# Performance work log

Hardware: AMD Instinct MI355X
Metric: run time of the kernel (lower is better)

The kernel has to match this reference:

```python
import jax, jax.numpy as jnp
import numpy as np

E, M, B, S = 1024, 256, 4, 2048
LN_EPS = 1e-5

def _l2norm(x):
    # F.normalize(p=2, dim=-1, eps=1e-12)
    n = jnp.linalg.norm(x, axis=-1, keepdims=True)
    return x / jnp.maximum(n, 1e-12)

def _layernorm(x, g, b):
    mu = jnp.mean(x, axis=-1, keepdims=True)
    var = jnp.var(x, axis=-1, keepdims=True)
    return (x - mu) * jax.lax.rsqrt(var + LN_EPS) * g + b

def setup_inputs() -> dict:
    key = jax.random.key(0)
    ks = jax.random.split(key, 16)
    s = 0.02
    inp = {
        'x': jax.random.normal(ks[0], (B, S, E), jnp.float32),
        'memory': jnp.zeros((B, M, M), jnp.float32),
        'w_k': jax.random.normal(ks[1], (M, E), jnp.float32) * s,
        'b_k': jnp.zeros((M,), jnp.float32),
        'w_q': jax.random.normal(ks[2], (M, E), jnp.float32) * s,
        'b_q': jnp.zeros((M,), jnp.float32),
        'w_v': jax.random.normal(ks[3], (M, E), jnp.float32) * s,
        'b_v': jnp.zeros((M,), jnp.float32),
        'w_out': jax.random.normal(ks[4], (E, M), jnp.float32) * s,
        'b_out': jnp.zeros((E,), jnp.float32),
        'w_gw': jax.random.normal(ks[5], (1, E), jnp.float32) * s,
        'b_gw': jnp.full((1,), -2.0, jnp.float32),
        'w_gf': jax.random.normal(ks[6], (1, E), jnp.float32) * s,
        'b_gf': jnp.full((1,), 2.0, jnp.float32),
        'ln1_g': jnp.ones((E,), jnp.float32),
        'ln1_b': jnp.zeros((E,), jnp.float32),
        'ln2_g': jnp.ones((E,), jnp.float32),
        'ln2_b': jnp.zeros((E,), jnp.float32),
        'w_f1': jax.random.normal(ks[7], (4 * E, E), jnp.float32) * s,
        'b_f1': jnp.zeros((4 * E,), jnp.float32),
        'w_f2': jax.random.normal(ks[8], (E, 4 * E), jnp.float32) * s,
        'b_f2': jnp.zeros((E,), jnp.float32),
    }
    return inp

def reference(x, memory, w_k, b_k, w_q, b_q, w_v, b_v, w_out, b_out,
              w_gw, b_gw, w_gf, b_gf, ln1_g, ln1_b, ln2_g, ln2_b,
              w_f1, b_f1, w_f2, b_f2):
    xn = _layernorm(x, ln1_g, ln1_b)                      # [B,S,E]
    k_all = _l2norm(xn @ w_k.T + b_k)                     # [B,S,M]
    q_all = _l2norm(xn @ w_q.T + b_q)                     # [B,S,M]
    v_all = jnp.tanh(xn @ w_v.T + b_v)                    # [B,S,M]
    beta_all = jax.nn.sigmoid(xn @ w_gw.T + b_gw)         # [B,S,1]
    decay_all = jax.nn.sigmoid(xn @ w_gf.T + b_gf)        # [B,S,1]

    def step(mem, inps):
        k, q, v, beta, decay = inps                       # k,q,v:[B,M]; beta,decay:[B,1]
        readout = jnp.einsum('bij,bj->bi', mem, q)        # read BEFORE update
        assoc = v[:, :, None] * k[:, None, :]             # [B,M,M] outer product
        mem = decay[:, :, None] * mem + beta[:, :, None] * assoc
        return mem, readout

    seq = (jnp.swapaxes(k_all, 0, 1), jnp.swapaxes(q_all, 0, 1),
           jnp.swapaxes(v_all, 0, 1), jnp.swapaxes(beta_all, 0, 1),
           jnp.swapaxes(decay_all, 0, 1))
    new_memory, readouts = jax.lax.scan(step, memory, seq)  # readouts: [S,B,M]
    stacked = jnp.swapaxes(readouts, 0, 1)                  # [B,S,M]
    mixer_out = stacked @ w_out.T + b_out                   # [B,S,E]

    x = x + mixer_out
    h = _layernorm(x, ln2_g, ln2_b)
    ffn = jax.nn.gelu(h @ w_f1.T + b_f1, approximate=False) @ w_f2.T + b_f2
    x = x + ffn
    return (x, new_memory)
```

## Files before the change

### kernel.cpp

```cpp
#include <hip/hip_runtime.h>
#include <stdint.h>

#define E_DIM 1024
#define M_DIM 256
#define B_DIM 4
#define S_DIM 2048
#define NTOK  8192
#define CHUNK 64
#define NCHUNK 32
#define NCB   128

typedef unsigned short u16;
typedef unsigned int   u32;
typedef __attribute__((ext_vector_type(8))) short short8;
typedef __attribute__((ext_vector_type(4))) float floatx4;

#define OFF_WKQV   ((size_t)0)
#define OFF_WOUT   ((size_t)1572864)
#define OFF_WF1    ((size_t)2097152)
#define OFF_WF2    ((size_t)10485760)
#define OFF_BKQV   ((size_t)18874368)
#define OFF_BETA   ((size_t)18877440)
#define OFF_DECAY  ((size_t)18910208)
#define OFF_P      ((size_t)18942976)
#define OFF_WW     ((size_t)18976256)
#define OFF_ABUF   ((size_t)19009024)
#define OFF_XN     ((size_t)21106176)
#define OFF_KQV    ((size_t)37883392)
#define OFF_T      ((size_t)63049216)
#define OFF_STATES ((size_t)96603648)
#define OFF_RO     ((size_t)130158080)
#define OFF_H      OFF_XN
#define OFF_Y1     OFF_T
#define OFF_G      OFF_STATES

__device__ __forceinline__ u16 f2bf(float f) {
    union { float f; u32 u; } a; a.f = f;
    u32 u = a.u;
    return (u16)((u + 0x7fffu + ((u >> 16) & 1u)) >> 16);
}
__device__ __forceinline__ u32 pack2bf(float a, float b) {
    return (u32)f2bf(a) | ((u32)f2bf(b) << 16);
}
__device__ __forceinline__ float sigmoidf_(float x) { return 1.0f / (1.0f + expf(-x)); }

__device__ __forceinline__ void gload_lds16(const u16* g, u16* l) {
    __builtin_amdgcn_global_load_lds((const __attribute__((address_space(1))) void*)g,
                                     (__attribute__((address_space(3))) void*)l, 16, 0, 0);
}

__device__ __forceinline__ int sw_slot(int idx) {
    return ((idx & 3) ^ ((idx >> 3) & 3)) * 8;
}
__device__ __forceinline__ int sw_read(int row, int kc) {
    return row * 32 + ((kc ^ ((row >> 1) & 3)) << 3);
}

__device__ __forceinline__ void block_reduce_2(float& a, float& b, float* red, int t) {
#pragma unroll
    for (int o = 32; o > 0; o >>= 1) { a += __shfl_xor(a, o); b += __shfl_xor(b, o); }
    if ((t & 63) == 0) { red[t >> 6] = a; red[4 + (t >> 6)] = b; }
    __syncthreads();
    a = red[0] + red[1] + red[2] + red[3];
    b = red[4] + red[5] + red[6] + red[7];
    __syncthreads();
}

__global__ void f2bf4_kernel(const float4* __restrict__ in, uint2* __restrict__ out, int n4) {
    int i = blockIdx.x * 256 + threadIdx.x;
    if (i < n4) {
        float4 v = in[i];
        uint2 o; o.x = pack2bf(v.x, v.y); o.y = pack2bf(v.z, v.w);
        out[i] = o;
    }
}
__global__ void pack_kqv_w(const float4* __restrict__ wk, const float4* __restrict__ wq,
                           const float4* __restrict__ wv, uint2* __restrict__ out) {
    int i = blockIdx.x * 256 + threadIdx.x;
    int sec = i >> 16;
    int off = i & 65535;
    const float4* src = (sec == 0) ? wk : ((sec == 1) ? wq : wv);
    float4 v = src[off];
    uint2 o; o.x = pack2bf(v.x, v.y); o.y = pack2bf(v.z, v.w);
    out[i] = o;
}
__global__ void pack_bias(const float* __restrict__ bk, const float* __restrict__ bq,
                          const float* __restrict__ bv, float* __restrict__ out) {
    int i = blockIdx.x * 256 + threadIdx.x;
    if (i < 256) out[i] = bk[i];
    else if (i < 512) out[i] = bq[i - 256];
    else out[i] = bv[i - 512];
}

__global__ __launch_bounds__(256) void ln1_gates(
    const float* __restrict__ x, const float* __restrict__ g, const float* __restrict__ b,
    const float* __restrict__ wgw, const float* __restrict__ bgw,
    const float* __restrict__ wgf, const float* __restrict__ bgf,
    u16* __restrict__ xn, float* __restrict__ beta, float* __restrict__ decay)
{
    __shared__ float red[8];
    const int row = blockIdx.x;
    const int t = threadIdx.x;
    const float4 v = ((const float4*)(x + (size_t)row * E_DIM))[t];
    float s  = v.x + v.y + v.z + v.w;
    float ss = v.x * v.x + v.y * v.y + v.z * v.z + v.w * v.w;
    block_reduce_2(s, ss, red, t);
    const float mean = s * (1.0f / E_DIM);
    const float var  = ss * (1.0f / E_DIM) - mean * mean;
    const float rstd = rsqrtf(var + 1e-5f);
    const float4 gg = ((const float4*)g)[t];
    const float4 bb = ((const float4*)b)[t];
    float4 xnv;
    xnv.x = (v.x - mean) * rstd * gg.x + bb.x;
    xnv.y = (v.y - mean) * rstd * gg.y + bb.y;
    xnv.z = (v.z - mean) * rstd * gg.z + bb.z;
    xnv.w = (v.w - mean) * rstd * gg.w + bb.w;
    uint2 o; o.x = pack2bf(xnv.x, xnv.y); o.y = pack2bf(xnv.z, xnv.w);
    ((uint2*)(xn + (size_t)row * E_DIM))[t] = o;
    const float4 w1 = ((const float4*)wgw)[t];
    const float4 w2 = ((const float4*)wgf)[t];
    float dg = xnv.x * w1.x + xnv.y * w1.y + xnv.z * w1.z + xnv.w * w1.w;
    float df = xnv.x * w2.x + xnv.y * w2.y + xnv.z * w2.z + xnv.w * w2.w;
    block_reduce_2(dg, df, red, t);
    if (t == 0) {
        beta[row]  = sigmoidf_(dg + bgw[0]);
        decay[row] = sigmoidf_(df + bgf[0]);
    }
}

__global__ __launch_bounds__(256) void ln2_kernel(
    const float* __restrict__ y1, const float* __restrict__ g, const float* __restrict__ b,
    u16* __restrict__ h)
{
    __shared__ float red[8];
    const int row = blockIdx.x;
    const int t = threadIdx.x;
    const float4 v = ((const float4*)(y1 + (size_t)row * E_DIM))[t];
    float s  = v.x + v.y + v.z + v.w;
    float ss = v.x * v.x + v.y * v.y + v.z * v.z + v.w * v.w;
    block_reduce_2(s, ss, red, t);
    const float mean = s * (1.0f / E_DIM);
    const float var  = ss * (1.0f / E_DIM) - mean * mean;
    const float rstd = rsqrtf(var + 1e-5f);
    const float4 gg = ((const float4*)g)[t];
    const float4 bb = ((const float4*)b)[t];
    float4 xnv;
    xnv.x = (v.x - mean) * rstd * gg.x + bb.x;
    xnv.y = (v.y - mean) * rstd * gg.y + bb.y;
    xnv.z = (v.z - mean) * rstd * gg.z + bb.z;
    xnv.w = (v.w - mean) * rstd * gg.w + bb.w;
    uint2 o; o.x = pack2bf(xnv.x, xnv.y); o.y = pack2bf(xnv.z, xnv.w);
    ((uint2*)(h + (size_t)row * E_DIM))[t] = o;
}

__global__ __launch_bounds__(256) void kqv_act(float* __restrict__ kqv) {
    __shared__ float red[8];
    const int row = blockIdx.x;
    const int t = threadIdx.x;
    float* p = kqv + (size_t)row * 768;
    float kv = p[t], qv = p[256 + t], vv = p[512 + t];
    float sk = kv * kv, sq = qv * qv;
    block_reduce_2(sk, sq, red, t);
    float nk = fmaxf(sqrtf(sk), 1e-12f);
    float nq = fmaxf(sqrtf(sq), 1e-12f);
    p[t]       = kv / nk;
    p[256 + t] = qv / nq;
    p[512 + t] = tanhf(vv);
}

__global__ void chunk_prep(const float* __restrict__ beta, const float* __restrict__ decay,
                           float* __restrict__ P, float* __restrict__ ww) {
    int cb = blockIdx.x;
    int b = cb >> 5, c = cb & 31;
    int tb = b * S_DIM + c * CHUNK;
    int j = threadIdx.x;
    __shared__ float d[64], bt[64], Ps[65];
    d[j]  = decay[tb + j];
    bt[j] = beta[tb + j];
    __syncthreads();
    if (j == 0) {
        float p = 1.0f; Ps[0] = 1.0f;
        for (int i = 0; i < 64; i++) { p *= d[i]; Ps[i + 1] = p; }
    }
    __syncthreads();
    P[cb * 65 + j] = Ps[j];
    if (j == 0) P[cb * 65 + 64] = Ps[64];
    ww[cb * 64 + j] = bt[j] / Ps[j + 1];
}

__global__ __launch_bounds__(256) void t_kernel(const float* __restrict__ kqv,
                                                const float* __restrict__ P,
                                                const float* __restrict__ ww,
                                                float* __restrict__ T) {
    int cb = blockIdx.y;
    int tile = blockIdx.x;
    int r0 = (tile >> 2) * 64, c0 = (tile & 3) * 64;
    int b = cb >> 5, c = cb & 31;
    int tb = b * S_DIM + c * CHUNK;
    float p64 = P[cb * 65 + 64];
    __shared__ float Vs[64][65], Ks[64][65];
    int t = threadIdx.x;
#pragma unroll
    for (int i = 0; i < 16; i++) {
        int idx = t + i * 256; int j = idx >> 6, col = idx & 63;
        float sc = ww[cb * 64 + j] * p64;
        Vs[j][col] = kqv[(size_t)(tb + j) * 768 + 512 + r0 + col] * sc;
        Ks[j][col] = kqv[(size_t)(tb + j) * 768 + 0   + c0 + col];
    }
    __syncthreads();
    int tr = t >> 4, tc = t & 15;
    float a[4][4] = {};
    for (int j = 0; j < 64; j++) {
        float vv[4], kk[4];
#pragma unroll
        for (int r = 0; r < 4; r++)  vv[r] = Vs[j][tr * 4 + r];
#pragma unroll
        for (int cc = 0; cc < 4; cc++) kk[cc] = Ks[j][tc * 4 + cc];
#pragma unroll
        for (int r = 0; r < 4; r++)
#pragma unroll
            for (int cc = 0; cc < 4; cc++) a[r][cc] += vv[r] * kk[cc];
    }
#pragma unroll
    for (int r = 0; r < 4; r++)
#pragma unroll
        for (int cc = 0; cc < 4; cc++)
            T[(size_t)cb * 65536 + (size_t)(r0 + tr * 4 + r) * 256 + (c0 + tc * 4 + cc)] = a[r][cc];
}

__global__ void mem_scan(const float* __restrict__ mem0, const float* __restrict__ T,
                         const float* __restrict__ P, float* __restrict__ states,
                         float* __restrict__ memOut) {
    int gid = blockIdx.x * 256 + threadIdx.x;
    int b = gid >> 16; int e = gid & 65535;
    float s = mem0[gid];
    for (int c = 0; c < NCHUNK; c++) {
        int cb = b * NCHUNK + c;
        states[(size_t)cb * 65536 + e] = s;
        s = P[cb * 65 + 64] * s + T[(size_t)cb * 65536 + e];
    }
    memOut[gid] = s;
}

__global__ __launch_bounds__(256) void qk_attn(const float* __restrict__ kqv,
                                               const float* __restrict__ P,
                                               const float* __restrict__ ww,
                                               float* __restrict__ Abuf) {
    int cb = blockIdx.x;
    int b = cb >> 5, c = cb & 31;
    int tb = b * S_DIM + c * CHUNK;
    __shared__ float Qs[64][65], Ks[64][65];
    int t = threadIdx.x;
    int tr = t >> 4, tc = t & 15;
    float acc[4][4] = {};
    for (int kt = 0; kt < 4; kt++) {
        __syncthreads();
#pragma unroll
        for (int i = 0; i < 16; i++) {
            int idx = t + i * 256; int rr = idx >> 6, cc2 = idx & 63;
            Qs[rr][cc2] = kqv[(size_t)(tb + rr) * 768 + 256 + kt * 64 + cc2];
            Ks[rr][cc2] = kqv[(size_t)(tb + rr) * 768 + 0   + kt * 64 + cc2];
        }
        __syncthreads();
        for (int kk = 0; kk < 64; kk++) {
            float qq[4], kx[4];
#pragma unroll
            for (int r = 0; r < 4; r++)  qq[r] = Qs[tr * 4 + r][kk];
#pragma unroll
            for (int cc = 0; cc < 4; cc++) kx[cc] = Ks[tc * 4 + cc][kk];
#pragma unroll
            for (int r = 0; r < 4; r++)
#pragma unroll
                for (int cc = 0; cc < 4; cc++) acc[r][cc] += qq[r] * kx[cc];
        }
    }
#pragma unroll
    for (int r = 0; r < 4; r++) {
#pragma unroll
        for (int cc = 0; cc < 4; cc++) {
            int i = tr * 4 + r, j = tc * 4 + cc;
            float v = (j < i) ? acc[r][cc] * (P[cb * 65 + i] * ww[cb * 64 + j]) : 0.0f;
            Abuf[(size_t)cb * 4096 + i * 64 + j] = v;
        }
    }
}

__global__ __launch_bounds__(256) void readout_k(const float* __restrict__ kqv,
                                                 const float* __restrict__ Abuf,
                                                 const float* __restrict__ states,
                                                 const float* __restrict__ P,
                                                 u16* __restrict__ ro) {
    int cb = blockIdx.y;
    int rt = blockIdx.x;
    int b = cb >> 5, c = cb & 31;
    int tb = b * S_DIM + c * CHUNK;
    int r0 = rt * 64;
    __shared__ float As[64][65], Vs[64][65], Qs[64][65], Ms[64][65];
    int t = threadIdx.x;
    int tr = t >> 4, tc = t & 15;
#pragma unroll
    for (int i = 0; i < 16; i++) {
        int idx = t + i * 256; int rr = idx >> 6, cc2 = idx & 63;
        As[rr][cc2] = Abuf[(size_t)cb * 4096 + rr * 64 + cc2];
        Vs[rr][cc2] = kqv[(size_t)(tb + rr) * 768 + 512 + r0 + cc2];
    }
    __syncthreads();
    float acc[4][4] = {};
    for (int j = 0; j < 64; j++) {
        float aa[4], vv[4];
#pragma unroll
        for (int r = 0; r < 4; r++)  aa[r] = As[tr * 4 + r][j];
#pragma unroll
        for (int cc = 0; cc < 4; cc++) vv[cc] = Vs[j][tc * 4 + cc];
#pragma unroll
        for (int r = 0; r < 4; r++)
#pragma unroll
            for (int cc = 0; cc < 4; cc++) acc[r][cc] += aa[r] * vv[cc];
    }
    float acc2[4][4] = {};
    for (int kt = 0; kt < 4; kt++) {
        __syncthreads();
#pragma unroll
        for (int i = 0; i < 16; i++) {
            int idx = t + i * 256; int rr = idx >> 6, cc2 = idx & 63;
            Qs[rr][cc2] = kqv[(size_t)(tb + rr) * 768 + 256 + kt * 64 + cc2];
            Ms[rr][cc2] = states[(size_t)cb * 65536 + (size_t)(r0 + rr) * 256 + kt * 64 + cc2];
        }
        __syncthreads();
        for (int kk = 0; kk < 64; kk++) {
            float qq[4], mm[4];
#pragma unroll
            for (int r = 0; r < 4; r++)  qq[r] = Qs[tr * 4 + r][kk];
#pragma unroll
            for (int cc = 0; cc < 4; cc++) mm[cc] = Ms[tc * 4 + cc][kk];
#pragma unroll
            for (int r = 0; r < 4; r++)
#pragma unroll
                for (int cc = 0; cc < 4; cc++) acc2[r][cc] += qq[r] * mm[cc];
        }
    }
#pragma unroll
    for (int r = 0; r < 4; r++) {
#pragma unroll
        for (int cc = 0; cc < 4; cc++) {
            int i = tr * 4 + r;
            float val = acc[r][cc] + P[cb * 65 + i] * acc2[r][cc];
            ro[(size_t)(tb + i) * 256 + r0 + tc * 4 + cc] = f2bf(val);
        }
    }
}

#define EPI_BIAS  0
#define EPI_RESID 1
#define EPI_GELU  2

template<int EPI, int BM>
__global__ __launch_bounds__(256) void gemm_bt(
    const u16* __restrict__ A, int lda,
    const u16* __restrict__ B, int ldb,
    const float* __restrict__ bias,
    const float* __restrict__ resid,
    float* __restrict__ outF, u16* __restrict__ outB,
    int ldc, int K)
{
    constexpr int MI = BM / 32;
    __shared__ u16 As[2][BM * 32];
    __shared__ u16 Bs[2][128 * 32];
    const int t = threadIdx.x;
    const int lane = t & 63;
    const int w = t >> 6;
    const int waveM = (w >> 1) * (BM / 2);
    const int waveN = (w & 1) * 64;
    const int m0 = blockIdx.y * BM;
    const int n0 = blockIdx.x * 128;

    const int sr = t >> 2, scw = sw_slot(t);
    const u16* Ag0 = A + (size_t)(m0 + sr) * lda + scw;
    const u16* Ag1 = A + (size_t)(m0 + 64 + sr) * lda + scw;
    const u16* Bg0 = B + (size_t)(n0 + sr) * ldb + scw;
    const u16* Bg1 = B + (size_t)(n0 + 64 + sr) * ldb + scw;

    floatx4 acc[MI][4] = {};

    const int kc = lane >> 4;
    const int rsel = lane & 15;
    const int NK = K >> 5;

    gload_lds16(Ag0, As[0] + t * 8);
    if (BM == 128) gload_lds16(Ag1, As[0] + (t + 256) * 8);
    gload_lds16(Bg0, Bs[0] + t * 8);
    gload_lds16(Bg1, Bs[0] + (t + 256) * 8);

    for (int kt = 0; kt < NK; kt++) {
        __syncthreads();
        const int cur = kt & 1;
        if (kt + 1 < NK) {
            const int kof = (kt + 1) * 32;
            gload_lds16(Ag0 + kof, As[cur ^ 1] + t * 8);
            if (BM == 128) gload_lds16(Ag1 + kof, As[cur ^ 1] + (t + 256) * 8);
            gload_lds16(Bg0 + kof, Bs[cur ^ 1] + t * 8);
            gload_lds16(Bg1 + kof, Bs[cur ^ 1] + (t + 256) * 8);
        }
        short8 af[MI], bfr[4];
#pragma unroll
        for (int i = 0; i < MI; i++)
            af[i] = *(const short8*)(As[cur] + sw_read(waveM + i * 16 + rsel, kc));
#pragma unroll
        for (int j = 0; j < 4; j++)
            bfr[j] = *(const short8*)(Bs[cur] + sw_read(waveN + j * 16 + rsel, kc));
#pragma unroll
        for (int i = 0; i < MI; i++)
#pragma unroll
            for (int j = 0; j < 4; j++)
                acc[i][j] = __builtin_amdgcn_mfma_f32_16x16x32_bf16(af[i], bfr[j], acc[i][j], 0, 0, 0);
    }

    const int rbase = (lane >> 4) * 4;
#pragma unroll
    for (int i = 0; i < MI; i++) {
#pragma unroll
        for (int j = 0; j < 4; j++) {
            const int col = n0 + waveN + j * 16 + rsel;
            const float bv = bias[col];
#pragma unroll
            for (int r = 0; r < 4; r++) {
                const int row = m0 + waveM + i * 16 + rbase + r;
                const size_t oidx = (size_t)row * ldc + col;
                float v = acc[i][j][r] + bv;
                if (EPI == EPI_BIAS) {
                    outF[oidx] = v;
                } else if (EPI == EPI_RESID) {
                    outF[oidx] = v + resid[oidx];
                } else {
                    float gl = 0.5f * v * (1.0f + erff(v * 0.70710678118654752f));
                    outB[oidx] = f2bf(gl);
                }
            }
        }
    }
}

extern "C" void kernel_launch(void* const* d_in, const int* in_sizes, int n_in,
                              void* d_out, int out_size, void* d_ws, size_t ws_size,
                              hipStream_t stream) {
    const float* x     = (const float*)d_in[0];
    const float* mem0  = (const float*)d_in[1];
    const float* w_k   = (const float*)d_in[2];
    const float* b_k   = (const float*)d_in[3];
    const float* w_q   = (const float*)d_in[4];
    const float* b_q   = (const float*)d_in[5];
    const float* w_v   = (const float*)d_in[6];
    const float* b_v   = (const float*)d_in[7];
    const float* w_out = (const float*)d_in[8];
    const float* b_out = (const float*)d_in[9];
    const float* w_gw  = (const float*)d_in[10];
    const float* b_gw  = (const float*)d_in[11];
    const float* w_gf  = (const float*)d_in[12];
    const float* b_gf  = (const float*)d_in[13];
    const float* ln1g  = (const float*)d_in[14];
    const float* ln1b  = (const float*)d_in[15];
    const float* ln2g  = (const float*)d_in[16];
    const float* ln2b  = (const float*)d_in[17];
    const float* w_f1  = (const float*)d_in[18];
    const float* b_f1  = (const float*)d_in[19];
    const float* w_f2  = (const float*)d_in[20];
    const float* b_f2  = (const float*)d_in[21];

    char* ws = (char*)d_ws;
    u16*   wkqv  = (u16*)(ws + OFF_WKQV);
    u16*   wout  = (u16*)(ws + OFF_WOUT);
    u16*   wf1   = (u16*)(ws + OFF_WF1);
    u16*   wf2   = (u16*)(ws + OFF_WF2);
    float* bkqv  = (float*)(ws + OFF_BKQV);
    float* beta  = (float*)(ws + OFF_BETA);
    float* decay = (float*)(ws + OFF_DECAY);
    float* P     = (float*)(ws + OFF_P);
    float* ww    = (float*)(ws + OFF_WW);
    float* Abuf  = (float*)(ws + OFF_ABUF);
    u16*   xn    = (u16*)(ws + OFF_XN);
    float* kqv   = (float*)(ws + OFF_KQV);
    float* T     = (float*)(ws + OFF_T);
    float* states= (float*)(ws + OFF_STATES);
    u16*   ro    = (u16*)(ws + OFF_RO);
    u16*   h     = (u16*)(ws + OFF_H);
    float* y1    = (float*)(ws + OFF_Y1);
    u16*   g     = (u16*)(ws + OFF_G);

    float* out_x   = (float*)d_out;
    float* out_mem = out_x + (size_t)NTOK * E_DIM;

    pack_kqv_w<<<768, 256, 0, stream>>>((const float4*)w_k, (const float4*)w_q,
                                        (const float4*)w_v, (uint2*)wkqv);
    f2bf4_kernel<<<256, 256, 0, stream>>>((const float4*)w_out, (uint2*)wout, 1024 * 256 / 4);
    f2bf4_kernel<<<4096, 256, 0, stream>>>((const float4*)w_f1, (uint2*)wf1, 4096 * 1024 / 4);
    f2bf4_kernel<<<4096, 256, 0, stream>>>((const float4*)w_f2, (uint2*)wf2, 1024 * 4096 / 4);
    pack_bias<<<3, 256, 0, stream>>>(b_k, b_q, b_v, bkqv);

    ln1_gates<<<NTOK, 256, 0, stream>>>(x, ln1g, ln1b, w_gw, b_gw, w_gf, b_gf, xn, beta, decay);

    gemm_bt<EPI_BIAS, 64><<<dim3(6, 128), 256, 0, stream>>>(xn, 1024, wkqv, 1024, bkqv, nullptr,
                                                            kqv, nullptr, 768, 1024);
    kqv_act<<<NTOK, 256, 0, stream>>>(kqv);

    chunk_prep<<<NCB, 64, 0, stream>>>(beta, decay, P, ww);
    t_kernel<<<dim3(16, NCB), 256, 0, stream>>>(kqv, P, ww, T);
    mem_scan<<<1024, 256, 0, stream>>>(mem0, T, P, states, out_mem);
    qk_attn<<<NCB, 256, 0, stream>>>(kqv, P, ww, Abuf);
    readout_k<<<dim3(4, NCB), 256, 0, stream>>>(kqv, Abuf, states, P, ro);

    gemm_bt<EPI_RESID, 64><<<dim3(8, 128), 256, 0, stream>>>(ro, 256, wout, 256, b_out, x,
                                                             y1, nullptr, 1024, 256);
    ln2_kernel<<<NTOK, 256, 0, stream>>>(y1, ln2g, ln2b, h);
    gemm_bt<EPI_GELU, 128><<<dim3(32, 64), 256, 0, stream>>>(h, 1024, wf1, 1024, b_f1, nullptr,
                                                             nullptr, g, 4096, 1024);
    gemm_bt<EPI_RESID, 64><<<dim3(8, 128), 256, 0, stream>>>(g, 4096, wf2, 4096, b_f2, y1,
                                                             out_x, nullptr, 1024, 4096);
}
```

Measured before the change: 531.4 us.

## Split-K the KQV and FFN2 GEMMs with larger tiles and merge weight conversions

Fuses the five weight/bias conversion launches into one kernel. The KQV projection and the second FFN GEMM now use 128-row tiles and a split-K of 2 across blockIdx.z. The second partial sum goes to scratch and is added back later: in kqv_act, which also applies the bias, or in a new combine kernel for the FFN output. This keeps enough blocks in flight with the larger tiles, at the cost of extra partial-sum traffic through global memory and one more launch.

```diff
diff --git a/kernel.cpp b/kernel.cpp
--- a/kernel.cpp
+++ b/kernel.cpp
@@ -33,6 +33,7 @@
 #define OFF_H      OFF_XN
 #define OFF_Y1     OFF_T
 #define OFF_G      OFF_STATES
+#define OFF_P2     OFF_XN
 
 __device__ __forceinline__ u16 f2bf(float f) {
     union { float f; u32 u; } a; a.f = f;
@@ -66,30 +67,35 @@
     __syncthreads();
 }
 
-__global__ void f2bf4_kernel(const float4* __restrict__ in, uint2* __restrict__ out, int n4) {
-    int i = blockIdx.x * 256 + threadIdx.x;
-    if (i < n4) {
-        float4 v = in[i];
-        uint2 o; o.x = pack2bf(v.x, v.y); o.y = pack2bf(v.z, v.w);
-        out[i] = o;
-    }
-}
-__global__ void pack_kqv_w(const float4* __restrict__ wk, const float4* __restrict__ wq,
-                           const float4* __restrict__ wv, uint2* __restrict__ out) {
-    int i = blockIdx.x * 256 + threadIdx.x;
-    int sec = i >> 16;
-    int off = i & 65535;
-    const float4* src = (sec == 0) ? wk : ((sec == 1) ? wq : wv);
-    float4 v = src[off];
-    uint2 o; o.x = pack2bf(v.x, v.y); o.y = pack2bf(v.z, v.w);
-    out[i] = o;
-}
-__global__ void pack_bias(const float* __restrict__ bk, const float* __restrict__ bq,
-                          const float* __restrict__ bv, float* __restrict__ out) {
-    int i = blockIdx.x * 256 + threadIdx.x;
-    if (i < 256) out[i] = bk[i];
-    else if (i < 512) out[i] = bq[i - 256];
-    else out[i] = bv[i - 512];
+__device__ __forceinline__ uint2 cvt4(float4 v) {
+    uint2 o; o.x = pack2bf(v.x, v.y); o.y = pack2bf(v.z, v.w); return o;
+}
+__global__ void convert_weights(const float4* __restrict__ wk, const float4* __restrict__ wq,
+                                const float4* __restrict__ wv, const float4* __restrict__ wo,
+                                const float4* __restrict__ wf1in, const float4* __restrict__ wf2in,
+                                const float* __restrict__ bk, const float* __restrict__ bq,
+                                const float* __restrict__ bv,
+                                uint2* __restrict__ wkqv, uint2* __restrict__ wout,
+                                uint2* __restrict__ wf1, uint2* __restrict__ wf2,
+                                float* __restrict__ bkqv) {
+    int b = blockIdx.x, t = threadIdx.x;
+    if (b < 768) {
+        int i = b * 256 + t;
+        int sec = i >> 16, off = i & 65535;
+        const float4* s = (sec == 0) ? wk : ((sec == 1) ? wq : wv);
+        wkqv[i] = cvt4(s[off]);
+    } else if (b < 1024) {
+        int i = (b - 768) * 256 + t;
+        wout[i] = cvt4(wo[i]);
+    } else if (b < 5120) {
+        int i = (b - 1024) * 256 + t;
+        wf1[i] = cvt4(wf1in[i]);
+    } else if (b < 9216) {
+        int i = (b - 5120) * 256 + t;
+        wf2[i] = cvt4(wf2in[i]);
+    } else {
+        bkqv[t] = bk[t]; bkqv[256 + t] = bq[t]; bkqv[512 + t] = bv[t];
+    }
 }
 
 __global__ __launch_bounds__(256) void ln1_gates(
@@ -153,12 +159,17 @@
     ((uint2*)(h + (size_t)row * E_DIM))[t] = o;
 }
 
-__global__ __launch_bounds__(256) void kqv_act(float* __restrict__ kqv) {
+__global__ __launch_bounds__(256) void kqv_act(float* __restrict__ pA,
+                                               const float* __restrict__ pB,
+                                               const float* __restrict__ bias) {
     __shared__ float red[8];
     const int row = blockIdx.x;
     const int t = threadIdx.x;
-    float* p = kqv + (size_t)row * 768;
-    float kv = p[t], qv = p[256 + t], vv = p[512 + t];
+    float* p = pA + (size_t)row * 768;
+    const float* q = pB + (size_t)row * 768;
+    float kv = p[t]       + q[t]       + bias[t];
+    float qv = p[256 + t] + q[256 + t] + bias[256 + t];
+    float vv = p[512 + t] + q[512 + t] + bias[512 + t];
     float sk = kv * kv, sq = qv * qv;
     block_reduce_2(sk, sq, red, t);
     float nk = fmaxf(sqrtf(sk), 1e-12f);
@@ -350,9 +361,19 @@
     }
 }
 
-#define EPI_BIAS  0
-#define EPI_RESID 1
-#define EPI_GELU  2
+__global__ __launch_bounds__(256) void combine_k(float4* __restrict__ out,
+                                                 const float4* __restrict__ part) {
+    int i = blockIdx.x * 256 + threadIdx.x;
+    float4 a = out[i], b = part[i];
+    a.x += b.x; a.y += b.y; a.z += b.z; a.w += b.w;
+    out[i] = a;
+}
+
+#define EPI_BIAS   0
+#define EPI_RESID  1
+#define EPI_GELU   2
+#define EPI_SPART  3
+#define EPI_SRESID 4
 
 template<int EPI, int BM>
 __global__ __launch_bounds__(256) void gemm_bt(
@@ -361,7 +382,7 @@
     const float* __restrict__ bias,
     const float* __restrict__ resid,
     float* __restrict__ outF, u16* __restrict__ outB,
-    int ldc, int K)
+    int ldc, int K, float* __restrict__ part)
 {
     constexpr int MI = BM / 32;
     __shared__ u16 As[2][BM * 32];
@@ -373,12 +394,13 @@
     const int waveN = (w & 1) * 64;
     const int m0 = blockIdx.y * BM;
     const int n0 = blockIdx.x * 128;
+    const size_t koff = (size_t)blockIdx.z * K;
 
     const int sr = t >> 2, scw = sw_slot(t);
-    const u16* Ag0 = A + (size_t)(m0 + sr) * lda + scw;
-    const u16* Ag1 = A + (size_t)(m0 + 64 + sr) * lda + scw;
-    const u16* Bg0 = B + (size_t)(n0 + sr) * ldb + scw;
-    const u16* Bg1 = B + (size_t)(n0 + 64 + sr) * ldb + scw;
+    const u16* Ag0 = A + (size_t)(m0 + sr) * lda + koff + scw;
+    const u16* Ag1 = A + (size_t)(m0 + 64 + sr) * lda + koff + scw;
+    const u16* Bg0 = B + (size_t)(n0 + sr) * ldb + koff + scw;
+    const u16* Bg1 = B + (size_t)(n0 + 64 + sr) * ldb + koff + scw;
 
     floatx4 acc[MI][4] = {};
 
@@ -415,13 +437,16 @@
                 acc[i][j] = __builtin_amdgcn_mfma_f32_16x16x32_bf16(af[i], bfr[j], acc[i][j], 0, 0, 0);
     }
 
+    const bool zmain = (blockIdx.z == 0);
     const int rbase = (lane >> 4) * 4;
 #pragma unroll
     for (int i = 0; i < MI; i++) {
 #pragma unroll
         for (int j = 0; j < 4; j++) {
             const int col = n0 + waveN + j * 16 + rsel;
-            const float bv = bias[col];
+            float bv = 0.0f;
+            if (EPI == EPI_BIAS || EPI == EPI_RESID || EPI == EPI_GELU) bv = bias[col];
+            if (EPI == EPI_SRESID && zmain) bv = bias[col];
 #pragma unroll
             for (int r = 0; r < 4; r++) {
                 const int row = m0 + waveM + i * 16 + rbase + r;
@@ -431,9 +456,14 @@
                     outF[oidx] = v;
                 } else if (EPI == EPI_RESID) {
                     outF[oidx] = v + resid[oidx];
-                } else {
+                } else if (EPI == EPI_GELU) {
                     float gl = 0.5f * v * (1.0f + erff(v * 0.70710678118654752f));
                     outB[oidx] = f2bf(gl);
+                } else if (EPI == EPI_SPART) {
+                    (zmain ? outF : part)[oidx] = v;
+                } else {
+                    if (zmain) outF[oidx] = v + resid[oidx];
+                    else       part[oidx] = v;
                 }
             }
         }
@@ -479,28 +509,29 @@
     float* Abuf  = (float*)(ws + OFF_ABUF);
     u16*   xn    = (u16*)(ws + OFF_XN);
     float* kqv   = (float*)(ws + OFF_KQV);
+    float* kqvPB = (float*)(ws + OFF_T);
     float* T     = (float*)(ws + OFF_T);
     float* states= (float*)(ws + OFF_STATES);
     u16*   ro    = (u16*)(ws + OFF_RO);
     u16*   h     = (u16*)(ws + OFF_H);
     float* y1    = (float*)(ws + OFF_Y1);
     u16*   g     = (u16*)(ws + OFF_G);
+    float* p2    = (float*)(ws + OFF_P2);
 
     float* out_x   = (float*)d_out;
     float* out_mem = out_x + (size_t)NTOK * E_DIM;
 
-    pack_kqv_w<<<768, 256, 0, stream>>>((const float4*)w_k, (const float4*)w_q,
-                                        (const float4*)w_v, (uint2*)wkqv);
-    f2bf4_kernel<<<256, 256, 0, stream>>>((const float4*)w_out, (uint2*)wout, 1024 * 256 / 4);
-    f2bf4_kernel<<<4096, 256, 0, stream>>>((const float4*)w_f1, (uint2*)wf1, 4096 * 1024 / 4);
-    f2bf4_kernel<<<4096, 256, 0, stream>>>((const float4*)w_f2, (uint2*)wf2, 1024 * 4096 / 4);
-    pack_bias<<<3, 256, 0, stream>>>(b_k, b_q, b_v, bkqv);
+    convert_weights<<<9217, 256, 0, stream>>>(
+        (const float4*)w_k, (const float4*)w_q, (const float4*)w_v,
+        (const float4*)w_out, (const float4*)w_f1, (const float4*)w_f2,
+        b_k, b_q, b_v,
+        (uint2*)wkqv, (uint2*)wout, (uint2*)wf1, (uint2*)wf2, bkqv);
 
     ln1_gates<<<NTOK, 256, 0, stream>>>(x, ln1g, ln1b, w_gw, b_gw, w_gf, b_gf, xn, beta, decay);
 
-    gemm_bt<EPI_BIAS, 64><<<dim3(6, 128), 256, 0, stream>>>(xn, 1024, wkqv, 1024, bkqv, nullptr,
-                                                            kqv, nullptr, 768, 1024);
-    kqv_act<<<NTOK, 256, 0, stream>>>(kqv);
+    gemm_bt<EPI_SPART, 128><<<dim3(6, 64, 2), 256, 0, stream>>>(
+        xn, 1024, wkqv, 1024, nullptr, nullptr, kqv, nullptr, 768, 512, kqvPB);
+    kqv_act<<<NTOK, 256, 0, stream>>>(kqv, kqvPB, bkqv);
 
     chunk_prep<<<NCB, 64, 0, stream>>>(beta, decay, P, ww);
     t_kernel<<<dim3(16, NCB), 256, 0, stream>>>(kqv, P, ww, T);
@@ -508,11 +539,13 @@
     qk_attn<<<NCB, 256, 0, stream>>>(kqv, P, ww, Abuf);
     readout_k<<<dim3(4, NCB), 256, 0, stream>>>(kqv, Abuf, states, P, ro);
 
-    gemm_bt<EPI_RESID, 64><<<dim3(8, 128), 256, 0, stream>>>(ro, 256, wout, 256, b_out, x,
-                                                             y1, nullptr, 1024, 256);
+    gemm_bt<EPI_RESID, 64><<<dim3(8, 128), 256, 0, stream>>>(
+        ro, 256, wout, 256, b_out, x, y1, nullptr, 1024, 256, nullptr);
+
     ln2_kernel<<<NTOK, 256, 0, stream>>>(y1, ln2g, ln2b, h);
-    gemm_bt<EPI_GELU, 128><<<dim3(32, 64), 256, 0, stream>>>(h, 1024, wf1, 1024, b_f1, nullptr,
-                                                             nullptr, g, 4096, 1024);
-    gemm_bt<EPI_RESID, 64><<<dim3(8, 128), 256, 0, stream>>>(g, 4096, wf2, 4096, b_f2, y1,
-                                                             out_x, nullptr, 1024, 4096);
-}
+    gemm_bt<EPI_GELU, 128><<<dim3(32, 64), 256, 0, stream>>>(
+        h, 1024, wf1, 1024, b_f1, nullptr, nullptr, g, 4096, 1024, nullptr);
+    gemm_bt<EPI_SRESID, 128><<<dim3(8, 64, 2), 256, 0, stream>>>(
+        g, 4096, wf2, 4096, b_f2, y1, out_x, nullptr, 1024, 2048, p2);
+    combine_k<<<8192, 256, 0, stream>>>((float4*)out_x, (const float4*)p2);
+}
```

After: 544.2 us. +2.4%, slower.
